# Kernel optimization log

Hardware: AMD Instinct MI355X
Metric: run time of the kernel (lower is better)

The kernel has to match this reference:

```python
import jax, jax.numpy as jnp
import numpy as np

H, CH = 4, 16          # heads, hidden_features // heads
SLOPE = 0.2            # leaky_relu negative slope


def gat(x, W, a_src, a_dst):
    # x: (B, N, C); W: (hidden, C); a_src/a_dst: (H, CH)
    B, N, _ = x.shape
    h = (x @ W.T).reshape(B, N, H, CH)
    a1 = jnp.einsum('bnhc,hc->bnh', h, a_src)   # att_src scores
    a2 = jnp.einsum('bnhc,hc->bnh', h, a_dst)   # att_dst scores
    # torch: a1.unsqueeze(1) + a2.unsqueeze(2) -> (B, N, N, H)
    e = a1[:, None, :, :] + a2[:, :, None, :]
    e = jnp.transpose(e, (0, 3, 1, 2))          # (B, H, N, N)
    e = jnp.where(e >= 0, e, SLOPE * e)         # leaky_relu
    return jax.nn.softmax(e, axis=2)            # softmax over dim=2 as in torch


def pool(x, W1, b1, W2, b2):
    # diff-pool assignment: (B, N, K), then x' = S^T x -> (B, K, C)
    s = jax.nn.softmax(jax.nn.relu(x @ W1.T + b1) @ W2.T + b2, axis=-1)
    return jnp.einsum('bnk,bnc->bkc', s, x)


def fuse(att0, atts, lefts, rights):
    out = att0
    for a, l, r in zip(atts, lefts, rights):
        # left (H,J0,K) @ att (B,H,K,K) @ right (H,K,J0), broadcast over batch
        out = out + jnp.einsum('hjk,bhkl,hlm->bhjm', l, a, r)
    return out


def setup_inputs() -> dict:
    key = jax.random.key(0)
    ks = iter(jax.random.split(key, 40))
    n = lambda shape, s=0.1: jax.random.normal(next(ks), shape, dtype=jnp.float32) * s
    inp = {
        'src': n((64, 64, 64, 25), 1.0),
        'gat_lin': n((6, 64, 64)), 'gat_asrc': n((6, 4, 16)), 'gat_adst': n((6, 4, 16)),
        'sp0_W1': n((64, 64)), 'sp0_b1': jnp.zeros((64,), jnp.float32),
        'sp0_W2': n((12, 64)), 'sp0_b2': jnp.zeros((12,), jnp.float32),
        'sp1_W1': n((64, 64)), 'sp1_b1': jnp.zeros((64,), jnp.float32),
        'sp1_W2': n((5, 64)), 'sp1_b2': jnp.zeros((5,), jnp.float32),
        'tp0_W1': n((64, 64)), 'tp0_b1': jnp.zeros((64,), jnp.float32),
        'tp0_W2': n((32, 64)), 'tp0_b2': jnp.zeros((32,), jnp.float32),
        'tp1_W1': n((64, 64)), 'tp1_b1': jnp.zeros((64,), jnp.float32),
        'tp1_W2': n((12, 64)), 'tp1_b2': jnp.zeros((12,), jnp.float32),
        'sl0': n((4, 25, 12)), 'sr0': n((4, 12, 25)),
        'sl1': n((4, 25, 5)), 'sr1': n((4, 5, 25)),
        'tl0': n((4, 64, 32)), 'tr0': n((4, 32, 64)),
        'tl1': n((4, 64, 12)), 'tr1': n((4, 12, 64)),
    }
    return inp


def reference(src, gat_lin, gat_asrc, gat_adst,
              sp0_W1, sp0_b1, sp0_W2, sp0_b2, sp1_W1, sp1_b1, sp1_W2, sp1_b2,
              tp0_W1, tp0_b1, tp0_W2, tp0_b2, tp1_W1, tp1_b1, tp1_W2, tp1_b2,
              sl0, sr0, sl1, sr1, tl0, tr0, tl1, tr1):
    B, C, T, J = src.shape
    # ---- spatial branch: attention over joints per (batch, frame) ----
    xs = jnp.transpose(src, (0, 2, 3, 1)).reshape(B * T, J, C)
    a_s0 = gat(xs, gat_lin[0], gat_asrc[0], gat_adst[0])            # (BT,H,25,25)
    xs1 = pool(xs, sp0_W1, sp0_b1, sp0_W2, sp0_b2)                  # (BT,12,C)
    a_s1 = gat(xs1, gat_lin[1], gat_asrc[1], gat_adst[1])           # (BT,H,12,12)
    xs2 = pool(xs1, sp1_W1, sp1_b1, sp1_W2, sp1_b2)                 # (BT,5,C)
    a_s2 = gat(xs2, gat_lin[2], gat_asrc[2], gat_adst[2])           # (BT,H,5,5)
    s_fused = fuse(a_s0, [a_s1, a_s2], [sl0, sl1], [sr0, sr1])
    # ---- temporal branch: attention over frames per (batch, joint) ----
    xt = jnp.transpose(src, (0, 3, 2, 1)).reshape(B * J, T, C)
    a_t0 = gat(xt, gat_lin[3], gat_asrc[3], gat_adst[3])            # (BJ,H,64,64)
    xt1 = pool(xt, tp0_W1, tp0_b1, tp0_W2, tp0_b2)                  # (BJ,32,C)
    a_t1 = gat(xt1, gat_lin[4], gat_asrc[4], gat_adst[4])
    xt2 = pool(xt1, tp1_W1, tp1_b1, tp1_W2, tp1_b2)                 # (BJ,12,C)
    a_t2 = gat(xt2, gat_lin[5], gat_asrc[5], gat_adst[5])
    t_fused = fuse(a_t0, [a_t1, a_t2], [tl0, tl1], [tr0, tr1])
    return (s_fused.reshape(B, T, H, J, J), t_fused.reshape(B, J, H, T, T))
```

## Files before the change

### kernel.cpp

```cpp
#include <hip/hip_runtime.h>

#define DEVINL __device__ __forceinline__

DEVINL float leaky(float v) { return v >= 0.f ? v : 0.2f * v; }

typedef float v4f __attribute__((ext_vector_type(4)));

DEVINL void nt_store4(float* p, float4 v) {
    v4f q = {v.x, v.y, v.z, v.w};
    __builtin_nontemporal_store(q, (v4f*)p);
}

__global__ void wprep_kernel(const float* __restrict__ lin,
                             const float* __restrict__ asrc,
                             const float* __restrict__ adst,
                             float* __restrict__ w_out) {
    int idx = blockIdx.x * blockDim.x + threadIdx.x;
    if (idx >= 6 * 4 * 64) return;
    int c = idx & 63;
    int h = (idx >> 6) & 3;
    int k = idx >> 8;
    const float* L = lin + k * 64 * 64;
    float s1 = 0.f, s2 = 0.f;
    for (int e = 0; e < 16; ++e) {
        float w = L[(h * 16 + e) * 64 + c];
        s1 += w * asrc[(k * 4 + h) * 16 + e];
        s2 += w * adst[(k * 4 + h) * 16 + e];
    }
    w_out[(k * 2 + 0) * 256 + h * 64 + c] = s1;
    w_out[(k * 2 + 1) * 256 + h * 64 + c] = s2;
}

__global__ void wtrans_kernel(const float* __restrict__ s0, const float* __restrict__ s1,
                              const float* __restrict__ t0, const float* __restrict__ t1,
                              const float* __restrict__ s0w2, const float* __restrict__ s1w2,
                              const float* __restrict__ t0w2, const float* __restrict__ t1w2,
                              float* __restrict__ o) {
    int idx = blockIdx.x * 256 + threadIdx.x;
    if (idx < 16384) {
        int m = idx >> 12, r = idx & 4095, c = r >> 6, d = r & 63;
        const float* src = (m == 0) ? s0 : (m == 1) ? s1 : (m == 2) ? t0 : t1;
        o[idx] = src[d * 64 + c];
    } else if (idx < 16384 + 768) {
        int j = idx - 16384, c = j / 12, k = j - 12 * c;
        o[idx] = s0w2[k * 64 + c];
    } else if (idx < 17152 + 512) {
        int j = idx - 17152, c = j >> 3, k = j & 7;
        o[idx] = (k < 5) ? s1w2[k * 64 + c] : 0.f;
    } else if (idx < 17664 + 2048) {
        int j = idx - 17664, c = j >> 5, k = j & 31;
        o[idx] = t0w2[k * 64 + c];
    } else if (idx < 19712 + 768) {
        int j = idx - 19712, c = j / 12, k = j - 12 * c;
        o[idx] = t1w2[k * 64 + c];
    }
}

__global__ void xs_kernel(const float* __restrict__ src, float* __restrict__ xs) {
    int g = blockIdx.x;
    int b = g >> 6, t = g & 63;
    __shared__ float tile[64][26];
    const float* sp = src + b * 102400 + t * 25;
    for (int idx = threadIdx.x; idx < 64 * 25; idx += blockDim.x) {
        int c = idx / 25, j = idx - c * 25;
        tile[c][j] = sp[c * 1600 + j];
    }
    __syncthreads();
    float* op = xs + g * 25 * 64;
    for (int idx = threadIdx.x; idx < 25 * 64; idx += blockDim.x) {
        int j = idx >> 6, c = idx & 63;
        op[idx] = tile[c][j];
    }
}

__global__ void xt_kernel(const float* __restrict__ src, float* __restrict__ xt) {
    int g = blockIdx.x;
    int b = g / 25, j = g - b * 25;
    __shared__ float tile[64][65];
    const float* sp = src + b * 102400 + j;
    for (int idx = threadIdx.x; idx < 64 * 64; idx += blockDim.x) {
        int c = idx >> 6, t = idx & 63;
        tile[c][t] = sp[c * 1600 + t * 25];
    }
    __syncthreads();
    float* op = xt + g * 64 * 64;
    for (int idx = threadIdx.x; idx < 64 * 64; idx += blockDim.x) {
        int t = idx >> 6, c = idx & 63;
        op[idx] = tile[c][t];
    }
}

template <int N>
__global__ __launch_bounds__(256) void gat_kernel(
    const float* __restrict__ x,
    const float* __restrict__ w,
    float* __restrict__ att) {
    int g = blockIdx.x;
    const int tid = threadIdx.x;
    __shared__ float xlT[64][N + 1];
    __shared__ float wl[512];
    __shared__ float a1s[4 * N], a2s[4 * N];
    __shared__ float rE[4 * N], rF[4 * N], cE[4 * N], cF[4 * N];
    __shared__ float mxs[4];
    const float* xp = x + (size_t)g * N * 64;
    for (int idx = tid; idx < N * 64; idx += 256) {
        int n = idx >> 6, c = idx & 63;
        xlT[c][n] = xp[idx];
    }
    for (int idx = tid; idx < 512; idx += 256) wl[idx] = w[idx];
    __syncthreads();
    for (int idx = tid; idx < 8 * N; idx += 256) {
        int n = idx % N;
        int hh = (idx / N) & 3;
        int sd = idx / (4 * N);
        const float* wp = wl + sd * 256 + hh * 64;
        float acc = 0.f;
        #pragma unroll 8
        for (int c = 0; c < 64; ++c) acc += xlT[c][n] * wp[c];
        (sd == 0 ? a1s : a2s)[hh * N + n] = acc;
    }
    __syncthreads();
    if (tid < 4) {
        float m = -1e30f;
        for (int i = 0; i < N; ++i) m = fmaxf(m, a2s[tid * N + i]);
        mxs[tid] = m;
    }
    __syncthreads();
    for (int idx = tid; idx < 4 * N; idx += 256) {
        int hh = idx / N;
        float d = a2s[idx] - mxs[hh];
        rE[idx] = __expf(d);
        rF[idx] = __expf(0.2f * d);
    }
    __syncthreads();
    for (int idx = tid; idx < 4 * N; idx += 256) {
        int hh = idx / N;
        float a = a1s[idx], mx = mxs[hh];
        float mj = leaky(a + mx);
        float E = __expf(a + mx - mj);
        float F = __expf(0.2f * (a + mx) - mj);
        float S1 = 0.f, S2 = 0.f;
        for (int i = 0; i < N; ++i) {
            bool c = (a + a2s[hh * N + i] >= 0.f);
            S1 += c ? rE[hh * N + i] : 0.f;
            S2 += c ? 0.f : rF[hh * N + i];
        }
        float iv = 1.f / (E * S1 + F * S2);
        cE[idx] = E * iv;
        cF[idx] = F * iv;
    }
    __syncthreads();
    float* ob = att + (size_t)g * 4 * N * N;
    if constexpr ((N % 4) == 0) {
        constexpr int NF4 = N / 4;
        for (int idx = tid; idx < 4 * N * NF4; idx += 256) {
            int row = idx / NF4;
            int j0 = (idx - row * NF4) * 4;
            int hh = row / N;
            float4 q1 = *(const float4*)&a1s[hh * N + j0];
            float4 qE = *(const float4*)&cE[hh * N + j0];
            float4 qF = *(const float4*)&cF[hh * N + j0];
            float a2i = a2s[row];
            float rEi = rE[row], rFi = rF[row];
            float a1v[4] = {q1.x, q1.y, q1.z, q1.w};
            float ev[4] = {qE.x, qE.y, qE.z, qE.w};
            float fv[4] = {qF.x, qF.y, qF.z, qF.w};
            float r[4];
            #pragma unroll
            for (int c = 0; c < 4; ++c)
                r[c] = (a1v[c] + a2i >= 0.f) ? ev[c] * rEi : fv[c] * rFi;
            *(float4*)&ob[row * N + j0] = make_float4(r[0], r[1], r[2], r[3]);
        }
    } else {
        for (int idx = tid; idx < 4 * N * N; idx += 256) {
            int hh = idx / (N * N), rem = idx - hh * N * N;
            int i = rem / N, j = rem - i * N;
            bool cnd = (a1s[hh * N + j] + a2s[hh * N + i] >= 0.f);
            ob[idx] = cnd ? cE[hh * N + j] * rE[hh * N + i]
                          : cF[hh * N + j] * rF[hh * N + i];
        }
    }
}

template <int N, int K, int KP>
__global__ __launch_bounds__(256, 3) void pool_kernel(
    const float* __restrict__ x,
    const float* __restrict__ W1T,
    const float* __restrict__ b1,
    const float* __restrict__ W2T,
    const float* __restrict__ b2,
    float* __restrict__ xo) {
    constexpr int NP = (N + 3) & ~3;
    constexpr int LDN = NP + 1;
    __shared__ float xlT[64 * LDN];
    __shared__ float yT[64 * LDN];
    __shared__ float sT[KP * LDN];
    const int g = blockIdx.x, tid = threadIdx.x;
    const float* xp = x + (size_t)g * N * 64;
    for (int i4 = tid; i4 < N * 16; i4 += 256) {
        int n = i4 >> 4, c0 = (i4 & 15) << 2;
        float4 v = ((const float4*)xp)[i4];
        xlT[(c0 + 0) * LDN + n] = v.x;
        xlT[(c0 + 1) * LDN + n] = v.y;
        xlT[(c0 + 2) * LDN + n] = v.z;
        xlT[(c0 + 3) * LDN + n] = v.w;
    }
    if constexpr (NP > N) {
        for (int i = tid; i < 64 * (NP - N); i += 256) {
            int c = i / (NP - N), n = N + i % (NP - N);
            xlT[c * LDN + n] = 0.f;
        }
    }
    __syncthreads();
    constexpr int T1 = (NP / 4) * 16;
    if (tid < T1) {
        int d0 = (tid & 15) << 2, n0 = (tid >> 4) << 2;
        float acc[4][4] = {};
        #pragma unroll 4
        for (int c = 0; c < 64; ++c) {
            float4 w4 = *(const float4*)(W1T + c * 64 + d0);
            float wv[4] = {w4.x, w4.y, w4.z, w4.w};
            float xv[4];
            #pragma unroll
            for (int r = 0; r < 4; ++r) xv[r] = xlT[c * LDN + n0 + r];
            #pragma unroll
            for (int r = 0; r < 4; ++r)
                #pragma unroll
                for (int cc = 0; cc < 4; ++cc) acc[r][cc] += xv[r] * wv[cc];
        }
        float4 b4 = *(const float4*)(b1 + d0);
        float bb[4] = {b4.x, b4.y, b4.z, b4.w};
        #pragma unroll
        for (int r = 0; r < 4; ++r)
            #pragma unroll
            for (int cc = 0; cc < 4; ++cc)
                yT[(d0 + cc) * LDN + n0 + r] = fmaxf(acc[r][cc] + bb[cc], 0.f);
    }
    __syncthreads();
    constexpr int KG4 = KP / 4;
    constexpr int T2 = (NP / 4) * KG4;
    if (tid < T2) {
        int k0 = (tid % KG4) << 2, n0 = (tid / KG4) << 2;
        float acc[4][4] = {};
        #pragma unroll 4
        for (int d = 0; d < 64; ++d) {
            float4 w4 = *(const float4*)(W2T + d * KP + k0);
            float wv[4] = {w4.x, w4.y, w4.z, w4.w};
            float yv[4];
            #pragma unroll
            for (int r = 0; r < 4; ++r) yv[r] = yT[d * LDN + n0 + r];
            #pragma unroll
            for (int r = 0; r < 4; ++r)
                #pragma unroll
                for (int cc = 0; cc < 4; ++cc) acc[r][cc] += yv[r] * wv[cc];
        }
        #pragma unroll
        for (int cc = 0; cc < 4; ++cc) {
            int k = k0 + cc;
            float bb = (k < K) ? b2[k] : 0.f;
            #pragma unroll
            for (int r = 0; r < 4; ++r)
                sT[k * LDN + n0 + r] = (k < K) ? (acc[r][cc] + bb) : -1e30f;
        }
    }
    __syncthreads();
    if (tid < NP) {
        float m = -1e30f;
        #pragma unroll
        for (int k = 0; k < KP; ++k) m = fmaxf(m, sT[k * LDN + tid]);
        float sum = 0.f;
        float e[KP];
        #pragma unroll
        for (int k = 0; k < KP; ++k) { e[k] = __expf(sT[k * LDN + tid] - m); sum += e[k]; }
        float inv = 1.f / sum;
        #pragma unroll
        for (int k = 0; k < KP; ++k) sT[k * LDN + tid] = e[k] * inv;
    }
    __syncthreads();
    constexpr int KG2 = (K + 1) / 2;
    constexpr int T3 = KG2 * 16;
    if (tid < T3) {
        int k0 = (tid % KG2) * 2, c0 = (tid / KG2) * 4;
        float acc0[4] = {}, acc1[4] = {};
        #pragma unroll 4
        for (int n = 0; n < N; ++n) {
            float sv0 = sT[k0 * LDN + n];
            float sv1 = sT[(k0 + 1) * LDN + n];
            float xv[4];
            #pragma unroll
            for (int j = 0; j < 4; ++j) xv[j] = xlT[(c0 + j) * LDN + n];
            #pragma unroll
            for (int j = 0; j < 4; ++j) { acc0[j] += sv0 * xv[j]; acc1[j] += sv1 * xv[j]; }
        }
        float* op = xo + (size_t)g * K * 64;
        *(float4*)&op[k0 * 64 + c0] = make_float4(acc0[0], acc0[1], acc0[2], acc0[3]);
        if (k0 + 1 < K)
            *(float4*)&op[(k0 + 1) * 64 + c0] = make_float4(acc1[0], acc1[1], acc1[2], acc1[3]);
    }
}

__global__ __launch_bounds__(256, 5) void gatfuse_t(
    const float* __restrict__ x,
    const float* __restrict__ w,
    const float* __restrict__ A1g,
    const float* __restrict__ L1,
    const float* __restrict__ R1,
    const float* __restrict__ A2g,
    const float* __restrict__ L2,
    const float* __restrict__ R2,
    float* __restrict__ out)
{
    const int bid = blockIdx.x;
    const int g = (bid & 7) | ((bid >> 5) << 3);
    const int h = (bid >> 3) & 3;
    const int tid = threadIdx.x;
    __shared__ float t1T[32 * 64];
    __shared__ float t2T[12 * 64];
    __shared__ float r1l[32 * 64];
    __shared__ float r2l[12 * 64];
    __shared__ float A1[32 * 36];
    __shared__ float A2[12 * 13];
    __shared__ float a01[64], a02[64];
    __shared__ float rEs[64], rFs[64], cEs[64], cFs[64];

    if (tid < 128) {
        int t = tid & 63, sd = tid >> 6;
        const float4* xr = (const float4*)(x + (size_t)g * 4096 + t * 64);
        const float* wv = w + sd * 256 + h * 64;
        float acc = 0.f;
        #pragma unroll
        for (int q = 0; q < 16; ++q) {
            float4 xv = xr[q];
            float4 w4 = *(const float4*)(wv + q * 4);
            acc += xv.x * w4.x + xv.y * w4.y + xv.z * w4.z + xv.w * w4.w;
        }
        (sd == 0 ? a01 : a02)[t] = acc;
    } else {
        int u = tid - 128;
        const float* a1p = A1g + (size_t)(g * 4 + h) * 1024;
        #pragma unroll
        for (int q = 0; q < 8; ++q) {
            int idx = q * 128 + u;
            A1[(idx >> 5) * 36 + (idx & 31)] = a1p[idx];
        }
        const float* a2p = A2g + (size_t)(g * 4 + h) * 144;
        for (int idx = u; idx < 144; idx += 128) {
            int k = idx / 12, l = idx - k * 12;
            A2[k * 13 + l] = a2p[idx];
        }
        const float4* r1p = (const float4*)(R1 + (size_t)h * 2048);
        #pragma unroll
        for (int q = 0; q < 4; ++q) ((float4*)r1l)[q * 128 + u] = r1p[q * 128 + u];
        const float4* r2p = (const float4*)(R2 + (size_t)h * 768);
        for (int idx = u; idx < 192; idx += 128) ((float4*)r2l)[idx] = r2p[idx];
    }
    __syncthreads();

    if (tid < 64) {
        float mx = a02[0];
        for (int i = 1; i < 64; ++i) mx = fmaxf(mx, a02[i]);
        float d = a02[tid] - mx;
        rEs[tid] = __expf(d);
        rFs[tid] = __expf(0.2f * d);
        cEs[tid] = mx;
    } else {
        const int j = tid & 63, l0 = (tid >> 6) * 8;
        float lj[32];
        const float4* lp = (const float4*)(L1 + ((size_t)h * 64 + j) * 32);
        #pragma unroll
        for (int q = 0; q < 8; ++q) {
            float4 v = lp[q];
            lj[q * 4] = v.x; lj[q * 4 + 1] = v.y; lj[q * 4 + 2] = v.z; lj[q * 4 + 3] = v.w;
        }
        float acc8[8] = {};
        for (int k = 0; k < 32; ++k) {
            float lk = lj[k];
            float4 a4a = *(const float4*)&A1[k * 36 + l0];
            float4 a4b = *(const float4*)&A1[k * 36 + l0 + 4];
            acc8[0] += lk * a4a.x; acc8[1] += lk * a4a.y;
            acc8[2] += lk * a4a.z; acc8[3] += lk * a4a.w;
            acc8[4] += lk * a4b.x; acc8[5] += lk * a4b.y;
            acc8[6] += lk * a4b.z; acc8[7] += lk * a4b.w;
        }
        #pragma unroll
        for (int lo = 0; lo < 8; ++lo) t1T[(l0 + lo) * 64 + j] = acc8[lo];
    }
    __syncthreads();

    if (tid < 64) {
        float mx = cEs[tid];
        float a = a01[tid];
        float mj = leaky(a + mx);
        float E = __expf(a + mx - mj);
        float F = __expf(0.2f * (a + mx) - mj);
        float S1 = 0.f, S2 = 0.f;
        for (int i = 0; i < 64; ++i) {
            bool c = (a + a02[i] >= 0.f);
            S1 += c ? rEs[i] : 0.f;
            S2 += c ? 0.f : rFs[i];
        }
        float iv = 1.f / (E * S1 + F * S2);
        cEs[tid] = E * iv;
        cFs[tid] = F * iv;
    } else if (tid < 128) {
        const int j = tid & 63;
        float lj[32];
        const float4* lp = (const float4*)(L1 + ((size_t)h * 64 + j) * 32);
        #pragma unroll
        for (int q = 0; q < 8; ++q) {
            float4 v = lp[q];
            lj[q * 4] = v.x; lj[q * 4 + 1] = v.y; lj[q * 4 + 2] = v.z; lj[q * 4 + 3] = v.w;
        }
        float acc8[8] = {};
        for (int k = 0; k < 32; ++k) {
            float lk = lj[k];
            float4 a4a = *(const float4*)&A1[k * 36];
            float4 a4b = *(const float4*)&A1[k * 36 + 4];
            acc8[0] += lk * a4a.x; acc8[1] += lk * a4a.y;
            acc8[2] += lk * a4a.z; acc8[3] += lk * a4a.w;
            acc8[4] += lk * a4b.x; acc8[5] += lk * a4b.y;
            acc8[6] += lk * a4b.z; acc8[7] += lk * a4b.w;
        }
        #pragma unroll
        for (int lo = 0; lo < 8; ++lo) t1T[lo * 64 + j] = acc8[lo];
    } else {
        const int j = tid & 63, lb = ((tid >> 6) - 2) * 6;
        float lj2[12];
        const float4* lp2 = (const float4*)(L2 + ((size_t)h * 64 + j) * 12);
        #pragma unroll
        for (int q = 0; q < 3; ++q) {
            float4 v = lp2[q];
            lj2[q * 4] = v.x; lj2[q * 4 + 1] = v.y;
            lj2[q * 4 + 2] = v.z; lj2[q * 4 + 3] = v.w;
        }
        #pragma unroll
        for (int lo = 0; lo < 6; ++lo) {
            int l = lb + lo;
            float acc = 0.f;
            #pragma unroll
            for (int k = 0; k < 12; ++k) acc += lj2[k] * A2[k * 13 + l];
            t2T[l * 64 + j] = acc;
        }
    }
    __syncthreads();

    const int i0 = (tid >> 4) << 2, m0 = (tid & 15) << 2;
    float acc[4][4];
    {
        float4 qa1 = *(const float4*)&a01[m0];
        float4 qcE = *(const float4*)&cEs[m0];
        float4 qcF = *(const float4*)&cFs[m0];
        float4 qa2 = *(const float4*)&a02[i0];
        float4 qrE = *(const float4*)&rEs[i0];
        float4 qrF = *(const float4*)&rFs[i0];
        float a1v[4] = {qa1.x, qa1.y, qa1.z, qa1.w};
        float ev[4] = {qcE.x, qcE.y, qcE.z, qcE.w};
        float fv[4] = {qcF.x, qcF.y, qcF.z, qcF.w};
        float a2v[4] = {qa2.x, qa2.y, qa2.z, qa2.w};
        float rev[4] = {qrE.x, qrE.y, qrE.z, qrE.w};
        float rfv[4] = {qrF.x, qrF.y, qrF.z, qrF.w};
        #pragma unroll
        for (int r = 0; r < 4; ++r)
            #pragma unroll
            for (int c = 0; c < 4; ++c)
                acc[r][c] = (a1v[c] + a2v[r] >= 0.f) ? ev[c] * rev[r]
                                                     : fv[c] * rfv[r];
    }
    #pragma unroll 8
    for (int l = 0; l < 32; ++l) {
        float4 t4 = *(const float4*)&t1T[l * 64 + i0];
        float4 r4 = *(const float4*)&r1l[l * 64 + m0];
        float tv[4] = {t4.x, t4.y, t4.z, t4.w};
        float rv[4] = {r4.x, r4.y, r4.z, r4.w};
        #pragma unroll
        for (int r = 0; r < 4; ++r)
            #pragma unroll
            for (int c = 0; c < 4; ++c) acc[r][c] += tv[r] * rv[c];
    }
    #pragma unroll 4
    for (int l = 0; l < 12; ++l) {
        float4 t4 = *(const float4*)&t2T[l * 64 + i0];
        float4 r4 = *(const float4*)&r2l[l * 64 + m0];
        float tv[4] = {t4.x, t4.y, t4.z, t4.w};
        float rv[4] = {r4.x, r4.y, r4.z, r4.w};
        #pragma unroll
        for (int r = 0; r < 4; ++r)
            #pragma unroll
            for (int c = 0; c < 4; ++c) acc[r][c] += tv[r] * rv[c];
    }
    float* op = out + ((size_t)g * 4 + h) * 4096;
    #pragma unroll
    for (int r = 0; r < 4; ++r)
        nt_store4(&op[(i0 + r) * 64 + m0],
                  make_float4(acc[r][0], acc[r][1], acc[r][2], acc[r][3]));
}

__global__ __launch_bounds__(256, 5) void gatfuse_s(
    const float* __restrict__ x,
    const float* __restrict__ w,
    const float* __restrict__ A1g,
    const float* __restrict__ L1,
    const float* __restrict__ R1,
    const float* __restrict__ A2g,
    const float* __restrict__ L2,
    const float* __restrict__ R2,
    float* __restrict__ out)
{
    const int g = blockIdx.x;
    const int tid = threadIdx.x;
    const int h = tid >> 6, t = tid & 63;
    __shared__ float xl[25 * 68];
    __shared__ float A1[4][12 * 13];
    __shared__ float A2[4][5 * 6];
    __shared__ float t1l[4][25 * 16];
    __shared__ float t2l[4][25 * 8];
    __shared__ float r1T[4][25 * 16];
    __shared__ float r2T[4][25 * 8];
    __shared__ float a01[4][25], a02[4][25];
    __shared__ float rE[4][25], rF[4][25], cE[4][25], cF[4][25];
    __shared__ float mxs[4];

    const float* xp = x + (size_t)g * 1600;
    for (int idx = tid; idx < 400; idx += 256) {
        int n = idx >> 4, c0 = (idx & 15) << 2;
        *(float4*)&xl[n * 68 + c0] = *(const float4*)(xp + n * 64 + c0);
    }
    const float* a1p = A1g + (size_t)(g * 4 + h) * 144;
    for (int idx = t; idx < 144; idx += 64) {
        int k = idx / 12, l = idx - k * 12;
        A1[h][k * 13 + l] = a1p[idx];
    }
    const float* a2p = A2g + (size_t)(g * 4 + h) * 25;
    if (t < 25) {
        int k = t / 5, l = t - (t / 5) * 5;
        A2[h][k * 6 + l] = a2p[t];
    }
    for (int idx = t; idx < 400; idx += 64) {
        int m = idx >> 4, l = idx & 15;
        r1T[h][idx] = (l < 12) ? R1[h * 300 + l * 25 + m] : 0.f;
    }
    for (int idx = t; idx < 200; idx += 64) {
        int m = idx >> 3, l = idx & 7;
        r2T[h][idx] = (l < 5) ? R2[h * 125 + l * 25 + m] : 0.f;
    }
    __syncthreads();

    if (t < 25) {
        const float* ws_ = w + h * 64;
        const float* wd_ = w + 256 + h * 64;
        const float* xr = &xl[t * 68];
        float s1 = 0.f, s2 = 0.f;
        #pragma unroll
        for (int c = 0; c < 64; c += 4) {
            float4 xv = *(const float4*)&xr[c];
            float4 w1 = *(const float4*)(ws_ + c);
            float4 w2 = *(const float4*)(wd_ + c);
            s1 += xv.x * w1.x + xv.y * w1.y + xv.z * w1.z + xv.w * w1.w;
            s2 += xv.x * w2.x + xv.y * w2.y + xv.z * w2.z + xv.w * w2.w;
        }
        a01[h][t] = s1;
        a02[h][t] = s2;
    }
    __syncthreads();

    if (t < 25) {
        float mx = a02[h][0];
        for (int i = 1; i < 25; ++i) mx = fmaxf(mx, a02[h][i]);
        if (t == 0) mxs[h] = mx;
        float d = a02[h][t] - mx;
        rE[h][t] = __expf(d);
        rF[h][t] = __expf(0.2f * d);
    } else if (t >= 32 && t < 57) {
        int i = t - 32;
        float lj[12];
        const float4* lp = (const float4*)(L1 + ((size_t)h * 25 + i) * 12);
        #pragma unroll
        for (int q = 0; q < 3; ++q) {
            float4 v = lp[q];
            lj[q * 4] = v.x; lj[q * 4 + 1] = v.y; lj[q * 4 + 2] = v.z; lj[q * 4 + 3] = v.w;
        }
        #pragma unroll
        for (int l = 0; l < 12; ++l) {
            float acc = 0.f;
            #pragma unroll
            for (int k = 0; k < 12; ++k) acc += lj[k] * A1[h][k * 13 + l];
            t1l[h][i * 16 + l] = acc;
        }
        #pragma unroll
        for (int l = 12; l < 16; ++l) t1l[h][i * 16 + l] = 0.f;
        float lj2[5];
        const float* lp2 = L2 + ((size_t)h * 25 + i) * 5;
        #pragma unroll
        for (int k = 0; k < 5; ++k) lj2[k] = lp2[k];
        #pragma unroll
        for (int l = 0; l < 5; ++l) {
            float acc = 0.f;
            #pragma unroll
            for (int k = 0; k < 5; ++k) acc += lj2[k] * A2[h][k * 6 + l];
            t2l[h][i * 8 + l] = acc;
        }
        #pragma unroll
        for (int l = 5; l < 8; ++l) t2l[h][i * 8 + l] = 0.f;
    }
    __syncthreads();

    if (t < 25) {
        float a = a01[h][t], mx = mxs[h];
        float mj = leaky(a + mx);
        float E = __expf(a + mx - mj);
        float F = __expf(0.2f * (a + mx) - mj);
        float S1 = 0.f, S2 = 0.f;
        for (int i = 0; i < 25; ++i) {
            bool c = (a + a02[h][i] >= 0.f);
            S1 += c ? rE[h][i] : 0.f;
            S2 += c ? 0.f : rF[h][i];
        }
        float iv = 1.f / (E * S1 + F * S2);
        cE[h][t] = E * iv;
        cF[h][t] = F * iv;
    }
    __syncthreads();

    float* op = out + ((size_t)g * 4 + h) * 625;
    for (int idx = t; idx < 625; idx += 64) {
        int i = idx / 25, m = idx - i * 25;
        bool cnd = (a01[h][m] + a02[h][i] >= 0.f);
        float val = cnd ? cE[h][m] * rE[h][i] : cF[h][m] * rF[h][i];
        const float* t1r = &t1l[h][i * 16];
        const float* r1c = &r1T[h][m * 16];
        #pragma unroll
        for (int q = 0; q < 4; ++q) {
            float4 tv = *(const float4*)&t1r[q * 4];
            float4 rv = *(const float4*)&r1c[q * 4];
            val += tv.x * rv.x + tv.y * rv.y + tv.z * rv.z + tv.w * rv.w;
        }
        const float* t2r = &t2l[h][i * 8];
        const float* r2c = &r2T[h][m * 8];
        #pragma unroll
        for (int q = 0; q < 2; ++q) {
            float4 tv = *(const float4*)&t2r[q * 4];
            float4 rv = *(const float4*)&r2c[q * 4];
            val += tv.x * rv.x + tv.y * rv.y + tv.z * rv.z + tv.w * rv.w;
        }
        __builtin_nontemporal_store(val, &op[idx]);
    }
}

extern "C" void kernel_launch(void* const* d_in, const int* in_sizes, int n_in,
                              void* d_out, int out_size, void* d_ws, size_t ws_size,
                              hipStream_t stream) {
    const float* src    = (const float*)d_in[0];
    const float* lin    = (const float*)d_in[1];
    const float* asrc   = (const float*)d_in[2];
    const float* adst   = (const float*)d_in[3];
    const float* sp0_W1 = (const float*)d_in[4];
    const float* sp0_b1 = (const float*)d_in[5];
    const float* sp0_W2 = (const float*)d_in[6];
    const float* sp0_b2 = (const float*)d_in[7];
    const float* sp1_W1 = (const float*)d_in[8];
    const float* sp1_b1 = (const float*)d_in[9];
    const float* sp1_W2 = (const float*)d_in[10];
    const float* sp1_b2 = (const float*)d_in[11];
    const float* tp0_W1 = (const float*)d_in[12];
    const float* tp0_b1 = (const float*)d_in[13];
    const float* tp0_W2 = (const float*)d_in[14];
    const float* tp0_b2 = (const float*)d_in[15];
    const float* tp1_W1 = (const float*)d_in[16];
    const float* tp1_b1 = (const float*)d_in[17];
    const float* tp1_W2 = (const float*)d_in[18];
    const float* tp1_b2 = (const float*)d_in[19];
    const float* sl0    = (const float*)d_in[20];
    const float* sr0    = (const float*)d_in[21];
    const float* sl1    = (const float*)d_in[22];
    const float* sr1    = (const float*)d_in[23];
    const float* tl0    = (const float*)d_in[24];
    const float* tr0    = (const float*)d_in[25];
    const float* tl1    = (const float*)d_in[26];
    const float* tr1    = (const float*)d_in[27];

    float* out_s = (float*)d_out;
    float* out_t = out_s + 10240000;

    float* ws   = (float*)d_ws;
    float* wbuf = ws;
    float* wT   = ws + 4096;
    float* region = ws + 24576;

    float* sp0_W1T = wT;
    float* sp1_W1T = wT + 4096;
    float* tp0_W1T = wT + 8192;
    float* tp1_W1T = wT + 12288;
    float* sp0_W2T = wT + 16384;
    float* sp1_W2T = wT + 17152;
    float* tp0_W2T = wT + 17664;
    float* tp1_W2T = wT + 19712;

    float* xs  = region;
    float* xs1 = xs + 6553600;
    float* xs2 = xs1 + 3145728;
    float* as1 = xs2 + 1310720;
    float* as2 = as1 + 2359296;
    float* xt  = region;
    float* xt1 = xt + 6553600;
    float* xt2 = xt1 + 3276800;
    float* at1 = xt2 + 1228800;
    float* at2 = at1 + 6553600;

    wprep_kernel<<<6, 256, 0, stream>>>(lin, asrc, adst, wbuf);
    wtrans_kernel<<<80, 256, 0, stream>>>(sp0_W1, sp1_W1, tp0_W1, tp1_W1,
                                          sp0_W2, sp1_W2, tp0_W2, tp1_W2, wT);

    xs_kernel<<<4096, 256, 0, stream>>>(src, xs);
    pool_kernel<25, 12, 12><<<4096, 256, 0, stream>>>(xs, sp0_W1T, sp0_b1, sp0_W2T, sp0_b2, xs1);
    gat_kernel<12><<<4096, 256, 0, stream>>>(xs1, wbuf + 1 * 512, as1);
    pool_kernel<12, 5, 8><<<4096, 256, 0, stream>>>(xs1, sp1_W1T, sp1_b1, sp1_W2T, sp1_b2, xs2);
    gat_kernel<5><<<4096, 256, 0, stream>>>(xs2, wbuf + 2 * 512, as2);
    gatfuse_s<<<4096, 256, 0, stream>>>(xs, wbuf + 0 * 512, as1, sl0, sr0, as2, sl1, sr1, out_s);

    xt_kernel<<<1600, 256, 0, stream>>>(src, xt);
    pool_kernel<64, 32, 32><<<1600, 256, 0, stream>>>(xt, tp0_W1T, tp0_b1, tp0_W2T, tp0_b2, xt1);
    gat_kernel<32><<<1600, 256, 0, stream>>>(xt1, wbuf + 4 * 512, at1);
    pool_kernel<32, 12, 12><<<1600, 256, 0, stream>>>(xt1, tp1_W1T, tp1_b1, tp1_W2T, tp1_b2, xt2);
    gat_kernel<12><<<1600, 256, 0, stream>>>(xt2, wbuf + 5 * 512, at2);
    gatfuse_t<<<6400, 256, 0, stream>>>(xt, wbuf + 3 * 512, at1, tl0, tr0, at2, tl1, tr1, out_t);
}
```

Baseline: 385.7 us.

## Simplify GAT softmax to direct exp form and read small attention from global

The gat kernel drops the factored rE/rF/cE/cF softmax tables and instead computes a per-column max and inverse sum, recomputing exp(leaky(e)-mj) per output element. The gatfuse_t kernel stops staging the A1/A2 attention matrices in shared memory, reads them straight from global memory (relying on cache), and raises the launch-bounds min-blocks hint from 5 to 6 to allow more resident blocks. The trade is more transcendental work per output and uncached-in-LDS global loads against less shared memory, fewer barriers and higher occupancy.

Result: slower. 428.4 us (+11.1%).

```diff
diff --git a/kernel.cpp b/kernel.cpp
--- a/kernel.cpp
+++ b/kernel.cpp
@@ -100,8 +100,8 @@
     __shared__ float xlT[64][N + 1];
     __shared__ float wl[512];
     __shared__ float a1s[4 * N], a2s[4 * N];
-    __shared__ float rE[4 * N], rF[4 * N], cE[4 * N], cF[4 * N];
     __shared__ float mxs[4];
+    __shared__ float mjs[4 * N], invs[4 * N];
     const float* xp = x + (size_t)g * N * 64;
     for (int idx = tid; idx < N * 64; idx += 256) {
         int n = idx >> 6, c = idx & 63;
@@ -128,26 +128,12 @@
     __syncthreads();
     for (int idx = tid; idx < 4 * N; idx += 256) {
         int hh = idx / N;
-        float d = a2s[idx] - mxs[hh];
-        rE[idx] = __expf(d);
-        rF[idx] = __expf(0.2f * d);
-    }
-    __syncthreads();
-    for (int idx = tid; idx < 4 * N; idx += 256) {
-        int hh = idx / N;
-        float a = a1s[idx], mx = mxs[hh];
-        float mj = leaky(a + mx);
-        float E = __expf(a + mx - mj);
-        float F = __expf(0.2f * (a + mx) - mj);
-        float S1 = 0.f, S2 = 0.f;
-        for (int i = 0; i < N; ++i) {
-            bool c = (a + a2s[hh * N + i] >= 0.f);
-            S1 += c ? rE[hh * N + i] : 0.f;
-            S2 += c ? 0.f : rF[hh * N + i];
-        }
-        float iv = 1.f / (E * S1 + F * S2);
-        cE[idx] = E * iv;
-        cF[idx] = F * iv;
+        float aj = a1s[idx];
+        float mj = leaky(aj + mxs[hh]);
+        float ssum = 0.f;
+        for (int i = 0; i < N; ++i) ssum += __expf(leaky(aj + a2s[hh * N + i]) - mj);
+        mjs[idx] = mj;
+        invs[idx] = 1.f / ssum;
     }
     __syncthreads();
     float* ob = att + (size_t)g * 4 * N * N;
@@ -158,26 +144,28 @@
             int j0 = (idx - row * NF4) * 4;
             int hh = row / N;
             float4 q1 = *(const float4*)&a1s[hh * N + j0];
-            float4 qE = *(const float4*)&cE[hh * N + j0];
-            float4 qF = *(const float4*)&cF[hh * N + j0];
+            float4 qm = *(const float4*)&mjs[hh * N + j0];
+            float4 qv = *(const float4*)&invs[hh * N + j0];
             float a2i = a2s[row];
-            float rEi = rE[row], rFi = rF[row];
             float a1v[4] = {q1.x, q1.y, q1.z, q1.w};
-            float ev[4] = {qE.x, qE.y, qE.z, qE.w};
-            float fv[4] = {qF.x, qF.y, qF.z, qF.w};
+            float mv[4] = {qm.x, qm.y, qm.z, qm.w};
+            float iv[4] = {qv.x, qv.y, qv.z, qv.w};
             float r[4];
             #pragma unroll
-            for (int c = 0; c < 4; ++c)
-                r[c] = (a1v[c] + a2i >= 0.f) ? ev[c] * rEi : fv[c] * rFi;
+            for (int c = 0; c < 4; ++c) {
+                float e = a1v[c] + a2i;
+                e = e >= 0.f ? e : 0.2f * e;
+                r[c] = __expf(e - mv[c]) * iv[c];
+            }
             *(float4*)&ob[row * N + j0] = make_float4(r[0], r[1], r[2], r[3]);
         }
     } else {
         for (int idx = tid; idx < 4 * N * N; idx += 256) {
             int hh = idx / (N * N), rem = idx - hh * N * N;
             int i = rem / N, j = rem - i * N;
-            bool cnd = (a1s[hh * N + j] + a2s[hh * N + i] >= 0.f);
-            ob[idx] = cnd ? cE[hh * N + j] * rE[hh * N + i]
-                          : cF[hh * N + j] * rF[hh * N + i];
+            float e = a1s[hh * N + j] + a2s[hh * N + i];
+            e = e >= 0.f ? e : 0.2f * e;
+            ob[idx] = __expf(e - mjs[hh * N + j]) * invs[hh * N + j];
         }
     }
 }
@@ -299,7 +287,7 @@
     }
 }
 
-__global__ __launch_bounds__(256, 5) void gatfuse_t(
+__global__ __launch_bounds__(256, 6) void gatfuse_t(
     const float* __restrict__ x,
     const float* __restrict__ w,
     const float* __restrict__ A1g,
@@ -318,10 +306,11 @@
     __shared__ float t2T[12 * 64];
     __shared__ float r1l[32 * 64];
     __shared__ float r2l[12 * 64];
-    __shared__ float A1[32 * 36];
-    __shared__ float A2[12 * 13];
     __shared__ float a01[64], a02[64];
     __shared__ float rEs[64], rFs[64], cEs[64], cFs[64];
+
+    const float* a1p = A1g + (size_t)(g * 4 + h) * 1024;
+    const float* a2p = A2g + (size_t)(g * 4 + h) * 144;
 
     if (tid < 128) {
         int t = tid & 63, sd = tid >> 6;
@@ -337,17 +326,6 @@
         (sd == 0 ? a01 : a02)[t] = acc;
     } else {
         int u = tid - 128;
-        const float* a1p = A1g + (size_t)(g * 4 + h) * 1024;
-        #pragma unroll
-        for (int q = 0; q < 8; ++q) {
-            int idx = q * 128 + u;
-            A1[(idx >> 5) * 36 + (idx & 31)] = a1p[idx];
-        }
-        const float* a2p = A2g + (size_t)(g * 4 + h) * 144;
-        for (int idx = u; idx < 144; idx += 128) {
-            int k = idx / 12, l = idx - k * 12;
-            A2[k * 13 + l] = a2p[idx];
-        }
         const float4* r1p = (const float4*)(R1 + (size_t)h * 2048);
         #pragma unroll
         for (int q = 0; q < 4; ++q) ((float4*)r1l)[q * 128 + u] = r1p[q * 128 + u];
@@ -375,8 +353,8 @@
         float acc8[8] = {};
         for (int k = 0; k < 32; ++k) {
             float lk = lj[k];
-            float4 a4a = *(const float4*)&A1[k * 36 + l0];
-            float4 a4b = *(const float4*)&A1[k * 36 + l0 + 4];
+            float4 a4a = *(const float4*)(a1p + k * 32 + l0);
+            float4 a4b = *(const float4*)(a1p + k * 32 + l0 + 4);
             acc8[0] += lk * a4a.x; acc8[1] += lk * a4a.y;
             acc8[2] += lk * a4a.z; acc8[3] += lk * a4a.w;
             acc8[4] += lk * a4b.x; acc8[5] += lk * a4b.y;
@@ -414,8 +392,8 @@
         float acc8[8] = {};
         for (int k = 0; k < 32; ++k) {
             float lk = lj[k];
-            float4 a4a = *(const float4*)&A1[k * 36];
-            float4 a4b = *(const float4*)&A1[k * 36 + 4];
+            float4 a4a = *(const float4*)(a1p + k * 32);
+            float4 a4b = *(const float4*)(a1p + k * 32 + 4);
             acc8[0] += lk * a4a.x; acc8[1] += lk * a4a.y;
             acc8[2] += lk * a4a.z; acc8[3] += lk * a4a.w;
             acc8[4] += lk * a4b.x; acc8[5] += lk * a4b.y;
@@ -438,7 +416,7 @@
             int l = lb + lo;
             float acc = 0.f;
             #pragma unroll
-            for (int k = 0; k < 12; ++k) acc += lj2[k] * A2[k * 13 + l];
+            for (int k = 0; k < 12; ++k) acc += lj2[k] * a2p[k * 12 + l];
             t2T[l * 64 + j] = acc;
         }
     }
```
